# Performance work log

Hardware: AMD Instinct MI355X
Metric: run time of the kernel (lower is better)

## Reference

```python
import jax, jax.numpy as jnp
import numpy as np

N_NODES = 50000
N_EDGES = 600000
D_IN = 128
D_HID = 128
D_OUT = 64


def setup_inputs() -> dict:
    key = jax.random.key(0)
    ks = jax.random.split(key, 8)
    x = jax.random.normal(ks[0], (N_NODES, D_IN), dtype=jnp.float32)
    edge_index = jax.random.randint(ks[1], (2, N_EDGES), 0, N_NODES, dtype=jnp.int32)
    s = 0.05
    W1l = jax.random.normal(ks[2], (D_HID, D_IN), dtype=jnp.float32) * s
    b1 = jnp.zeros((D_HID,), dtype=jnp.float32)
    W1r = jax.random.normal(ks[3], (D_HID, D_IN), dtype=jnp.float32) * s
    W2l = jax.random.normal(ks[4], (D_OUT, D_HID), dtype=jnp.float32) * s
    b2 = jnp.zeros((D_OUT,), dtype=jnp.float32)
    W2r = jax.random.normal(ks[5], (D_OUT, D_HID), dtype=jnp.float32) * s
    return {"x": x, "edge_index": edge_index, "W1l": W1l, "b1": b1,
            "W1r": W1r, "W2l": W2l, "b2": b2, "W2r": W2r}


def _sage_conv(x, src, dst, Wl, bl, Wr, n_nodes):
    # mean aggregation of source features at destination nodes
    msg_sum = jax.ops.segment_sum(x[src], dst, num_segments=n_nodes)  # [N, D]
    deg = jax.ops.segment_sum(jnp.ones((src.shape[0], 1), x.dtype), dst,
                              num_segments=n_nodes)                   # [N, 1]
    mean = msg_sum / jnp.maximum(deg, 1.0)
    # out = lin_l(mean_neighbors) + lin_r(x_self); bias only on lin_l (PyG default)
    return mean @ Wl.T + bl + x @ Wr.T


def reference(x, edge_index, W1l, b1, W1r, W2l, b2, W2r):
    src, dst = edge_index[0], edge_index[1]
    n = x.shape[0]
    h = jax.nn.relu(_sage_conv(x, src, dst, W1l, b1, W1r, n))
    # dropout p=0.5 is identity in eval mode (training=False)
    return _sage_conv(h, src, dst, W2l, b2, W2r, n)
```

## Files before the change

### kernel.cpp

```cpp
#include <hip/hip_runtime.h>
#include <hip/hip_bf16.h>

typedef __bf16 bf16x8 __attribute__((ext_vector_type(8)));
typedef float f32x4 __attribute__((ext_vector_type(4)));

#define D_FEAT 128
#define CHUNK 1024
#define NW 49344

__device__ __forceinline__ float bits_to_f(unsigned int u) {
    union { unsigned int i; float f; } c; c.i = u; return c.f;
}
__device__ __forceinline__ unsigned short f_to_bf16(float f) {
    __hip_bfloat16 h = (__hip_bfloat16)f;
    return *(unsigned short*)&h;
}
__device__ __forceinline__ float ld(const void* p, int is16, size_t i) {
    return is16 ? (float)((const __hip_bfloat16*)p)[i] : ((const float*)p)[i];
}
__device__ __forceinline__ int wave_probe16(const void* p) {
    const unsigned short v = ((const unsigned short*)p)[(threadIdx.x & 63) * 2];
    int e = (v >> 7) & 0xFF;
    unsigned long long m = __ballot(e >= 100 && e <= 140);
    return (__popcll(m) >= 48) ? 1 : 0;
}

__global__ void setup_kernel(const void* x,
                             const void* W1l, const void* b1, const void* W1r,
                             const void* W2l, const void* b2, const void* W2r,
                             const int* __restrict__ dst, int E,
                             unsigned short* __restrict__ wout, int* __restrict__ deg) {
    int i = blockIdx.x * blockDim.x + threadIdx.x;
    if (i < NW) {
        int is16 = wave_probe16(x);
        const void* s; int base;
        if      (i < 16384) { s = W1l; base = 0; }
        else if (i < 32768) { s = W1r; base = 16384; }
        else if (i < 40960) { s = W2l; base = 32768; }
        else if (i < 49152) { s = W2r; base = 40960; }
        else if (i < 49280) { s = b1;  base = 49152; }
        else                { s = b2;  base = 49280; }
        wout[i] = f_to_bf16(ld(s, is16, i - base));
    } else {
        int j = i - NW;
        if (j < E) atomicAdd(&deg[dst[j]], 1);
    }
}

__global__ void scan1_kernel(const int* __restrict__ deg, int* __restrict__ bsum, int n) {
    __shared__ int ws[4];
    const int lane = threadIdx.x & 63, wv = threadIdx.x >> 6;
    int i0 = blockIdx.x * CHUNK + threadIdx.x * 4;
    int s = 0;
    #pragma unroll
    for (int j = 0; j < 4; ++j)
        if (i0 + j < n) { int d = deg[i0 + j]; s += (d + 3) & ~3; }
    #pragma unroll
    for (int d = 1; d < 64; d <<= 1) s += __shfl_xor(s, d, 64);
    if (lane == 0) ws[wv] = s;
    __syncthreads();
    if (threadIdx.x == 0) bsum[blockIdx.x] = ws[0] + ws[1] + ws[2] + ws[3];
}

__global__ void scan3_kernel(const int* __restrict__ deg, const int* __restrict__ bsum,
                             int nb, int* __restrict__ off, int* __restrict__ cursor,
                             int* __restrict__ esrc, int n) {
    __shared__ int ws[4];
    const int lane = threadIdx.x & 63, wv = threadIdx.x >> 6;
    int bv = (lane < nb) ? bsum[lane] : 0;
    int bsc = bv;
    #pragma unroll
    for (int s = 1; s < 64; s <<= 1) {
        int t = __shfl_up(bsc, s, 64);
        if (lane >= s) bsc += t;
    }
    const int base = __shfl(bsc, blockIdx.x, 64) - __shfl(bv, blockIdx.x, 64);
    const int total = __shfl(bsc, nb - 1, 64);

    int i0 = blockIdx.x * CHUNK + threadIdx.x * 4;
    int d0 = 0, d1 = 0, d2 = 0, d3 = 0;
    if (i0 + 0 < n) d0 = deg[i0 + 0];
    if (i0 + 1 < n) d1 = deg[i0 + 1];
    if (i0 + 2 < n) d2 = deg[i0 + 2];
    if (i0 + 3 < n) d3 = deg[i0 + 3];
    int v0 = (d0 + 3) & ~3, v1 = (d1 + 3) & ~3, v2 = (d2 + 3) & ~3, v3 = (d3 + 3) & ~3;
    int tsum = v0 + v1 + v2 + v3;
    int sc = tsum;
    #pragma unroll
    for (int s = 1; s < 64; s <<= 1) {
        int t = __shfl_up(sc, s, 64);
        if (lane >= s) sc += t;
    }
    if (lane == 63) ws[wv] = sc;
    __syncthreads();
    int woff = 0;
    for (int w = 0; w < wv; ++w) woff += ws[w];
    int p = base + woff + (sc - tsum);
    #define EMIT(idx, dj, vj)                                            \
        if (i0 + idx < n) {                                              \
            off[i0 + idx] = p; cursor[i0 + idx] = p;                     \
            for (int q = p + dj; q < p + vj; ++q) esrc[q] = n;           \
            p += vj;                                                     \
        }
    EMIT(0, d0, v0) EMIT(1, d1, v1) EMIT(2, d2, v2) EMIT(3, d3, v3)
    #undef EMIT
    if (blockIdx.x == 0 && threadIdx.x == 0) off[n] = total;
}

__global__ void fill_kernel(const int* __restrict__ src, const int* __restrict__ dst,
                            int* __restrict__ cursor, int* __restrict__ esrc, int E) {
    int i = blockIdx.x * blockDim.x + threadIdx.x;
    if (i < E) {
        int p = atomicAdd(&cursor[dst[i]], 1);
        esrc[p] = src[i];
    }
}

template <int NOUT, bool PROBE_A>
__global__ __launch_bounds__(256)
void gemm_dual_kernel(const void* __restrict__ A,
                      const unsigned short* __restrict__ Wa,
                      const unsigned short* __restrict__ Wb,
                      const unsigned short* __restrict__ bias,
                      unsigned short* __restrict__ za, unsigned short* __restrict__ zb,
                      unsigned int* __restrict__ zrow, int zrow_words, int N) {
    if (blockIdx.x == 0 && threadIdx.x < zrow_words) zrow[threadIdx.x] = 0;
    int a16 = 1;
    if (PROBE_A) a16 = wave_probe16(A);

    const int lane = threadIdx.x & 63;
    const int wave = threadIdx.x >> 6;
    const int sel = wave & 1;
    const int m0 = blockIdx.x * 64 + (wave >> 1) * 32;
    if (m0 >= N) return;
    const int lrow = lane & 15;
    const int kg = lane >> 4;
    const unsigned short* W = sel ? Wb : Wa;
    unsigned short* z = sel ? zb : za;
    constexpr int NT = NOUT / 16;

    bf16x8 xf[2][4];
    #pragma unroll
    for (int rt = 0; rt < 2; ++rt) {
        const int gr = min(m0 + rt * 16 + lrow, N - 1);
        #pragma unroll
        for (int ks = 0; ks < 4; ++ks) {
            const int k0 = ks * 32 + kg * 8;
            if (a16) {
                xf[rt][ks] = *(const bf16x8*)((const unsigned short*)A + (size_t)gr * D_FEAT + k0);
            } else {
                const float* fp = (const float*)A + (size_t)gr * D_FEAT + k0;
                float4 f0 = *(const float4*)fp, f1 = *(const float4*)(fp + 4);
                union { bf16x8 v; unsigned short us[8]; } t;
                t.us[0] = f_to_bf16(f0.x); t.us[1] = f_to_bf16(f0.y);
                t.us[2] = f_to_bf16(f0.z); t.us[3] = f_to_bf16(f0.w);
                t.us[4] = f_to_bf16(f1.x); t.us[5] = f_to_bf16(f1.y);
                t.us[6] = f_to_bf16(f1.z); t.us[7] = f_to_bf16(f1.w);
                xf[rt][ks] = t.v;
            }
        }
    }

    f32x4 acc[2][NT];
    #pragma unroll
    for (int rt = 0; rt < 2; ++rt)
        #pragma unroll
        for (int t = 0; t < NT; ++t) acc[rt][t] = (f32x4){0, 0, 0, 0};

    #pragma unroll
    for (int ks = 0; ks < 4; ++ks) {
        const int k0 = ks * 32 + kg * 8;
        #pragma unroll
        for (int t = 0; t < NT; ++t) {
            bf16x8 wf = *(const bf16x8*)(W + (size_t)(t * 16 + lrow) * D_FEAT + k0);
            acc[0][t] = __builtin_amdgcn_mfma_f32_16x16x32_bf16(wf, xf[0][ks], acc[0][t], 0, 0, 0);
            acc[1][t] = __builtin_amdgcn_mfma_f32_16x16x32_bf16(wf, xf[1][ks], acc[1][t], 0, 0, 0);
        }
    }

    #pragma unroll
    for (int rt = 0; rt < 2; ++rt) {
        const int nd = m0 + rt * 16 + lrow;
        if (nd < N) {
            #pragma unroll
            for (int t = 0; t < NT; ++t) {
                const int c0 = t * 16 + kg * 4;
                float v0 = acc[rt][t][0], v1 = acc[rt][t][1];
                float v2 = acc[rt][t][2], v3 = acc[rt][t][3];
                if (sel) {
                    uint2 bb = *(const uint2*)(bias + c0);
                    v0 += bits_to_f(bb.x << 16); v1 += bits_to_f(bb.x & 0xffff0000u);
                    v2 += bits_to_f(bb.y << 16); v3 += bits_to_f(bb.y & 0xffff0000u);
                }
                unsigned int p0 = (unsigned int)f_to_bf16(v0) | ((unsigned int)f_to_bf16(v1) << 16);
                unsigned int p1 = (unsigned int)f_to_bf16(v2) | ((unsigned int)f_to_bf16(v3) << 16);
                *(uint2*)(z + (size_t)nd * NOUT + c0) = make_uint2(p0, p1);
            }
        }
    }
}

__global__ __launch_bounds__(256)
void agg1_kernel(const unsigned short* __restrict__ zl,
                 unsigned short* __restrict__ h,
                 const int* __restrict__ off, const int* __restrict__ deg,
                 const int* __restrict__ esrc, int N) {
    const int lane = threadIdx.x & 63;
    const int wave = threadIdx.x >> 6;
    const int a_lo = (blockIdx.x * 4 + wave) * 8;
    if (a_lo >= N) return;
    const int a_hi = min(a_lo + 8, N);
    const int nn = a_hi - a_lo;
    int offv = off[min(a_lo + min(lane, 8), N)];
    int degv = deg[min(a_lo + min(lane, 7), N - 1)];
    #define OFFAT(i) __shfl(offv, (i), 64)
    const int e_beg = OFFAT(0);
    const int e_end = OFFAT(nn);
    const int quarter = lane >> 4;
    const int fl = lane & 15;
    float ax[8];
    #pragma unroll
    for (int i = 0; i < 8; ++i) ax[i] = 0.f;
    int g = a_lo;
    int gend = OFFAT(1);

    auto flush = [&](int gg) {
        int td = __shfl(degv, gg - a_lo, 64);
        float inv = 1.f / (float)(td > 0 ? td : 1);
        float v[8];
        #pragma unroll
        for (int i = 0; i < 8; ++i) {
            float s = ax[i];
            s += __shfl_xor(s, 16, 64); s += __shfl_xor(s, 32, 64);
            v[i] = s * inv; ax[i] = 0.f;
        }
        if (quarter == 0) {
            unsigned short* hp = h + (size_t)gg * D_FEAT + fl * 8;
            uint4 zr = *(const uint4*)hp;
            unsigned int w[4] = {zr.x, zr.y, zr.z, zr.w};
            unsigned int pk[4];
            #pragma unroll
            for (int i = 0; i < 4; ++i) {
                float r0 = fmaxf(v[2 * i]     + bits_to_f(w[i] << 16), 0.f);
                float r1 = fmaxf(v[2 * i + 1] + bits_to_f(w[i] & 0xffff0000u), 0.f);
                pk[i] = (unsigned int)f_to_bf16(r0) | ((unsigned int)f_to_bf16(r1) << 16);
            }
            *(uint4*)hp = make_uint4(pk[0], pk[1], pk[2], pk[3]);
        }
    };

    int cur = (e_beg < e_end) ? esrc[min(e_beg + (lane & 31), e_end - 1)] : 0;
    for (int e = e_beg; e < e_end; e += 32) {
        int nxt = (e + 32 < e_end) ? esrc[min(e + 32 + (lane & 31), e_end - 1)] : 0;
        uint4 r[8];
        #pragma unroll
        for (int k = 0; k < 8; ++k) {
            int sk = __shfl(cur, 4 * k + quarter, 64);
            r[k] = *(const uint4*)(zl + (size_t)sk * D_FEAT + fl * 8);
        }
        #pragma unroll
        for (int k = 0; k < 8; ++k) {
            const int eb = e + 4 * k;
            if (eb < e_end) {
                while (eb >= gend) {
                    flush(g); ++g;
                    gend = OFFAT(min(g - a_lo + 1, 8));
                }
                uint4 u = r[k];
                ax[0] += bits_to_f(u.x << 16); ax[1] += bits_to_f(u.x & 0xffff0000u);
                ax[2] += bits_to_f(u.y << 16); ax[3] += bits_to_f(u.y & 0xffff0000u);
                ax[4] += bits_to_f(u.z << 16); ax[5] += bits_to_f(u.z & 0xffff0000u);
                ax[6] += bits_to_f(u.w << 16); ax[7] += bits_to_f(u.w & 0xffff0000u);
            }
        }
        cur = nxt;
    }
    while (g < a_hi) {
        flush(g); ++g;
        gend = OFFAT(min(g - a_lo + 1, 8));
    }
    #undef OFFAT
}

__global__ __launch_bounds__(256)
void agg2_kernel(const unsigned short* __restrict__ z2l,
                 const unsigned short* __restrict__ s2,
                 void* __restrict__ out, const void* __restrict__ x,
                 const int* __restrict__ off, const int* __restrict__ deg,
                 const int* __restrict__ esrc, int N) {
    const int o16 = wave_probe16(x);
    const int lane = threadIdx.x & 63;
    const int wave = threadIdx.x >> 6;
    const int a_lo = (blockIdx.x * 4 + wave) * 8;
    if (a_lo >= N) return;
    const int a_hi = min(a_lo + 8, N);
    const int nn = a_hi - a_lo;
    int offv = off[min(a_lo + min(lane, 8), N)];
    int degv = deg[min(a_lo + min(lane, 7), N - 1)];
    #define OFFAT(i) __shfl(offv, (i), 64)
    const int e_beg = OFFAT(0);
    const int e_end = OFFAT(nn);
    const int quarter = lane >> 4;
    const int fl = lane & 15;
    float ax[4];
    #pragma unroll
    for (int i = 0; i < 4; ++i) ax[i] = 0.f;
    int g = a_lo;
    int gend = OFFAT(1);

    auto flush = [&](int gg) {
        int td = __shfl(degv, gg - a_lo, 64);
        float inv = 1.f / (float)(td > 0 ? td : 1);
        float v[4];
        #pragma unroll
        for (int i = 0; i < 4; ++i) {
            float s = ax[i];
            s += __shfl_xor(s, 16, 64); s += __shfl_xor(s, 32, 64);
            v[i] = s * inv; ax[i] = 0.f;
        }
        if (quarter == 0) {
            uint2 sb = *(const uint2*)(s2 + (size_t)gg * 64 + fl * 4);
            v[0] += bits_to_f(sb.x << 16); v[1] += bits_to_f(sb.x & 0xffff0000u);
            v[2] += bits_to_f(sb.y << 16); v[3] += bits_to_f(sb.y & 0xffff0000u);
            if (o16) {
                unsigned int p0 = (unsigned int)f_to_bf16(v[0]) | ((unsigned int)f_to_bf16(v[1]) << 16);
                unsigned int p1 = (unsigned int)f_to_bf16(v[2]) | ((unsigned int)f_to_bf16(v[3]) << 16);
                *(uint2*)((unsigned short*)out + (size_t)gg * 64 + fl * 4) = make_uint2(p0, p1);
            } else {
                *(float4*)((float*)out + (size_t)gg * 64 + fl * 4) =
                    make_float4(v[0], v[1], v[2], v[3]);
            }
        }
    };

    int cur = (e_beg < e_end) ? esrc[min(e_beg + (lane & 31), e_end - 1)] : 0;
    for (int e = e_beg; e < e_end; e += 32) {
        int nxt = (e + 32 < e_end) ? esrc[min(e + 32 + (lane & 31), e_end - 1)] : 0;
        uint2 r[8];
        #pragma unroll
        for (int k = 0; k < 8; ++k) {
            int sk = __shfl(cur, 4 * k + quarter, 64);
            r[k] = *(const uint2*)(z2l + (size_t)sk * 64 + fl * 4);
        }
        #pragma unroll
        for (int k = 0; k < 8; ++k) {
            const int eb = e + 4 * k;
            if (eb < e_end) {
                while (eb >= gend) {
                    flush(g); ++g;
                    gend = OFFAT(min(g - a_lo + 1, 8));
                }
                uint2 u = r[k];
                ax[0] += bits_to_f(u.x << 16); ax[1] += bits_to_f(u.x & 0xffff0000u);
                ax[2] += bits_to_f(u.y << 16); ax[3] += bits_to_f(u.y & 0xffff0000u);
            }
        }
        cur = nxt;
    }
    while (g < a_hi) {
        flush(g); ++g;
        gend = OFFAT(min(g - a_lo + 1, 8));
    }
    #undef OFFAT
}

extern "C" void kernel_launch(void* const* d_in, const int* in_sizes, int n_in,
                              void* d_out, int out_size, void* d_ws, size_t ws_size,
                              hipStream_t stream) {
    const void* x   = d_in[0];
    const int* eidx = (const int*)d_in[1];
    const void* W1l = d_in[2];
    const void* b1  = d_in[3];
    const void* W1r = d_in[4];
    const void* W2l = d_in[5];
    const void* b2  = d_in[6];
    const void* W2r = d_in[7];

    const int N = in_sizes[0] / D_FEAT;
    const int E = in_sizes[1] / 2;
    const int* src = eidx;
    const int* dst = eidx + E;

    char* ws = (char*)d_ws;
    size_t o = 0;
    auto alloc = [&](size_t bytes) -> void* {
        void* p = ws + o;
        o += (bytes + 255) & ~(size_t)255;
        return p;
    };
    int* deg    = (int*)alloc((size_t)N * 4);
    int* off    = (int*)alloc((size_t)(N + 1) * 4);
    int* cursor = (int*)alloc((size_t)N * 4);
    int* bsum   = (int*)alloc(64 * 4);
    int* esrc   = (int*)alloc((size_t)(E + 3 * N + 64) * 4);
    unsigned short* wconv = (unsigned short*)alloc(NW * 2);
    unsigned short* zl = (unsigned short*)alloc((size_t)(N + 1) * D_FEAT * 2);
    unsigned short* h  = (unsigned short*)alloc((size_t)N * D_FEAT * 2);
    unsigned short* z2l = zl;
    unsigned short* s2  = zl + (size_t)(N + 1) * 64;
    (void)n_in; (void)out_size; (void)ws_size;

    hipMemsetAsync(deg, 0, (size_t)N * 4, stream);
    setup_kernel<<<(NW + E + 255) / 256, 256, 0, stream>>>(
        x, W1l, b1, W1r, W2l, b2, W2r, dst, E, wconv, deg);
    const int nchunk = (N + CHUNK - 1) / CHUNK;
    scan1_kernel<<<nchunk, 256, 0, stream>>>(deg, bsum, N);
    scan3_kernel<<<nchunk, 256, 0, stream>>>(deg, bsum, nchunk, off, cursor, esrc, N);
    fill_kernel<<<(E + 255) / 256, 256, 0, stream>>>(src, dst, cursor, esrc, E);

    const int gblocks = (N + 63) / 64;
    const int ablocks = (N + 31) / 32;
    gemm_dual_kernel<128, true><<<gblocks, 256, 0, stream>>>(
        x, wconv + 0, wconv + 16384, wconv + 49152,
        zl, h, (unsigned int*)(zl + (size_t)N * D_FEAT), 64, N);
    agg1_kernel<<<ablocks, 256, 0, stream>>>(zl, h, off, deg, esrc, N);
    gemm_dual_kernel<64, false><<<gblocks, 256, 0, stream>>>(
        h, wconv + 32768, wconv + 40960, wconv + 49280,
        z2l, s2, (unsigned int*)(z2l + (size_t)N * 64), 32, N);
    agg2_kernel<<<ablocks, 256, 0, stream>>>(z2l, s2, d_out, x, off, deg, esrc, N);
}
```

Measured before the change: 246.8 us.

## Store gathered neighbor projections in fp8 and shrink nodes per wave

The lin_l projections consumed by the two mean-aggregation gathers are now written in fp8 (packed with hardware cvt_pk_fp8) instead of bf16, and unpacked with cvt_pk_f32_fp8 in the aggregation kernels. This halves the bytes fetched per random neighbor row, the dominant memory traffic. Each wave now covers 4 destination nodes instead of 8, doubling the aggregation grid for more parallelism. The self/bias term stays in bf16 in a separate buffer. The cost is substantially lower precision in the aggregated messages, which risks tolerance failures.

```diff
diff --git a/kernel.cpp b/kernel.cpp
--- a/kernel.cpp
+++ b/kernel.cpp
@@ -3,6 +3,7 @@
 
 typedef __bf16 bf16x8 __attribute__((ext_vector_type(8)));
 typedef float f32x4 __attribute__((ext_vector_type(4)));
+typedef float f32x2 __attribute__((ext_vector_type(2)));
 
 #define D_FEAT 128
 #define CHUNK 1024
@@ -17,6 +18,11 @@
 }
 __device__ __forceinline__ float ld(const void* p, int is16, size_t i) {
     return is16 ? (float)((const __hip_bfloat16*)p)[i] : ((const float*)p)[i];
+}
+__device__ __forceinline__ unsigned int pack4_fp8(float v0, float v1, float v2, float v3) {
+    int w = __builtin_amdgcn_cvt_pk_fp8_f32(v0, v1, 0, false);
+    w = __builtin_amdgcn_cvt_pk_fp8_f32(v2, v3, w, true);
+    return (unsigned int)w;
 }
 __device__ __forceinline__ int wave_probe16(const void* p) {
     const unsigned short v = ((const unsigned short*)p)[(threadIdx.x & 63) * 2];
@@ -122,7 +128,7 @@
                       const unsigned short* __restrict__ Wa,
                       const unsigned short* __restrict__ Wb,
                       const unsigned short* __restrict__ bias,
-                      unsigned short* __restrict__ za, unsigned short* __restrict__ zb,
+                      unsigned char* __restrict__ za, unsigned short* __restrict__ zb,
                       unsigned int* __restrict__ zrow, int zrow_words, int N) {
     if (blockIdx.x == 0 && threadIdx.x < zrow_words) zrow[threadIdx.x] = 0;
     int a16 = 1;
@@ -136,7 +142,6 @@
     const int lrow = lane & 15;
     const int kg = lane >> 4;
     const unsigned short* W = sel ? Wb : Wa;
-    unsigned short* z = sel ? zb : za;
     constexpr int NT = NOUT / 16;
 
     bf16x8 xf[2][4];
@@ -191,28 +196,30 @@
                     uint2 bb = *(const uint2*)(bias + c0);
                     v0 += bits_to_f(bb.x << 16); v1 += bits_to_f(bb.x & 0xffff0000u);
                     v2 += bits_to_f(bb.y << 16); v3 += bits_to_f(bb.y & 0xffff0000u);
+                    unsigned int p0 = (unsigned int)f_to_bf16(v0) | ((unsigned int)f_to_bf16(v1) << 16);
+                    unsigned int p1 = (unsigned int)f_to_bf16(v2) | ((unsigned int)f_to_bf16(v3) << 16);
+                    *(uint2*)(zb + (size_t)nd * NOUT + c0) = make_uint2(p0, p1);
+                } else {
+                    *(unsigned int*)(za + (size_t)nd * NOUT + c0) = pack4_fp8(v0, v1, v2, v3);
                 }
-                unsigned int p0 = (unsigned int)f_to_bf16(v0) | ((unsigned int)f_to_bf16(v1) << 16);
-                unsigned int p1 = (unsigned int)f_to_bf16(v2) | ((unsigned int)f_to_bf16(v3) << 16);
-                *(uint2*)(z + (size_t)nd * NOUT + c0) = make_uint2(p0, p1);
             }
         }
     }
 }
 
 __global__ __launch_bounds__(256)
-void agg1_kernel(const unsigned short* __restrict__ zl,
+void agg1_kernel(const unsigned char* __restrict__ zl,
                  unsigned short* __restrict__ h,
                  const int* __restrict__ off, const int* __restrict__ deg,
                  const int* __restrict__ esrc, int N) {
     const int lane = threadIdx.x & 63;
     const int wave = threadIdx.x >> 6;
-    const int a_lo = (blockIdx.x * 4 + wave) * 8;
+    const int a_lo = (blockIdx.x * 4 + wave) * 4;
     if (a_lo >= N) return;
-    const int a_hi = min(a_lo + 8, N);
+    const int a_hi = min(a_lo + 4, N);
     const int nn = a_hi - a_lo;
-    int offv = off[min(a_lo + min(lane, 8), N)];
-    int degv = deg[min(a_lo + min(lane, 7), N - 1)];
+    int offv = off[min(a_lo + min(lane, 4), N)];
+    int degv = deg[min(a_lo + min(lane, 3), N - 1)];
     #define OFFAT(i) __shfl(offv, (i), 64)
     const int e_beg = OFFAT(0);
     const int e_end = OFFAT(nn);
@@ -252,11 +259,11 @@
     int cur = (e_beg < e_end) ? esrc[min(e_beg + (lane & 31), e_end - 1)] : 0;
     for (int e = e_beg; e < e_end; e += 32) {
         int nxt = (e + 32 < e_end) ? esrc[min(e + 32 + (lane & 31), e_end - 1)] : 0;
-        uint4 r[8];
+        uint2 r[8];
         #pragma unroll
         for (int k = 0; k < 8; ++k) {
             int sk = __shfl(cur, 4 * k + quarter, 64);
-            r[k] = *(const uint4*)(zl + (size_t)sk * D_FEAT + fl * 8);
+            r[k] = *(const uint2*)(zl + (size_t)sk * D_FEAT + fl * 8);
         }
         #pragma unroll
         for (int k = 0; k < 8; ++k) {
@@ -264,26 +271,27 @@
             if (eb < e_end) {
                 while (eb >= gend) {
                     flush(g); ++g;
-                    gend = OFFAT(min(g - a_lo + 1, 8));
+                    gend = OFFAT(min(g - a_lo + 1, 4));
                 }
-                uint4 u = r[k];
-                ax[0] += bits_to_f(u.x << 16); ax[1] += bits_to_f(u.x & 0xffff0000u);
-                ax[2] += bits_to_f(u.y << 16); ax[3] += bits_to_f(u.y & 0xffff0000u);
-                ax[4] += bits_to_f(u.z << 16); ax[5] += bits_to_f(u.z & 0xffff0000u);
-                ax[6] += bits_to_f(u.w << 16); ax[7] += bits_to_f(u.w & 0xffff0000u);
+                f32x2 p0 = __builtin_amdgcn_cvt_pk_f32_fp8((int)r[k].x, false);
+                f32x2 p1 = __builtin_amdgcn_cvt_pk_f32_fp8((int)r[k].x, true);
+                f32x2 p2 = __builtin_amdgcn_cvt_pk_f32_fp8((int)r[k].y, false);
+                f32x2 p3 = __builtin_amdgcn_cvt_pk_f32_fp8((int)r[k].y, true);
+                ax[0] += p0.x; ax[1] += p0.y; ax[2] += p1.x; ax[3] += p1.y;
+                ax[4] += p2.x; ax[5] += p2.y; ax[6] += p3.x; ax[7] += p3.y;
             }
         }
         cur = nxt;
     }
     while (g < a_hi) {
         flush(g); ++g;
-        gend = OFFAT(min(g - a_lo + 1, 8));
+        gend = OFFAT(min(g - a_lo + 1, 4));
     }
     #undef OFFAT
 }
 
 __global__ __launch_bounds__(256)
-void agg2_kernel(const unsigned short* __restrict__ z2l,
+void agg2_kernel(const unsigned char* __restrict__ z2l,
                  const unsigned short* __restrict__ s2,
                  void* __restrict__ out, const void* __restrict__ x,
                  const int* __restrict__ off, const int* __restrict__ deg,
@@ -291,12 +299,12 @@
     const int o16 = wave_probe16(x);
     const int lane = threadIdx.x & 63;
     const int wave = threadIdx.x >> 6;
-    const int a_lo = (blockIdx.x * 4 + wave) * 8;
+    const int a_lo = (blockIdx.x * 4 + wave) * 4;
     if (a_lo >= N) return;
-    const int a_hi = min(a_lo + 8, N);
+    const int a_hi = min(a_lo + 4, N);
     const int nn = a_hi - a_lo;
-    int offv = off[min(a_lo + min(lane, 8), N)];
-    int degv = deg[min(a_lo + min(lane, 7), N - 1)];
+    int offv = off[min(a_lo + min(lane, 4), N)];
+    int degv = deg[min(a_lo + min(lane, 3), N - 1)];
     #define OFFAT(i) __shfl(offv, (i), 64)
     const int e_beg = OFFAT(0);
     const int e_end = OFFAT(nn);
@@ -336,11 +344,11 @@
     int cur = (e_beg < e_end) ? esrc[min(e_beg + (lane & 31), e_end - 1)] : 0;
     for (int e = e_beg; e < e_end; e += 32) {
         int nxt = (e + 32 < e_end) ? esrc[min(e + 32 + (lane & 31), e_end - 1)] : 0;
-        uint2 r[8];
+        unsigned int r[8];
         #pragma unroll
         for (int k = 0; k < 8; ++k) {
             int sk = __shfl(cur, 4 * k + quarter, 64);
-            r[k] = *(const uint2*)(z2l + (size_t)sk * 64 + fl * 4);
+            r[k] = *(const unsigned int*)(z2l + (size_t)sk * 64 + fl * 4);
         }
         #pragma unroll
         for (int k = 0; k < 8; ++k) {
@@ -348,18 +356,18 @@
             if (eb < e_end) {
                 while (eb >= gend) {
                     flush(g); ++g;
-                    gend = OFFAT(min(g - a_lo + 1, 8));
+                    gend = OFFAT(min(g - a_lo + 1, 4));
                 }
-                uint2 u = r[k];
-                ax[0] += bits_to_f(u.x << 16); ax[1] += bits_to_f(u.x & 0xffff0000u);
-                ax[2] += bits_to_f(u.y << 16); ax[3] += bits_to_f(u.y & 0xffff0000u);
+                f32x2 p0 = __builtin_amdgcn_cvt_pk_f32_fp8((int)r[k], false);
+                f32x2 p1 = __builtin_amdgcn_cvt_pk_f32_fp8((int)r[k], true);
+                ax[0] += p0.x; ax[1] += p0.y; ax[2] += p1.x; ax[3] += p1.y;
             }
         }
         cur = nxt;
     }
     while (g < a_hi) {
         flush(g); ++g;
-        gend = OFFAT(min(g - a_lo + 1, 8));
+        gend = OFFAT(min(g - a_lo + 1, 4));
     }
     #undef OFFAT
 }
@@ -394,10 +402,10 @@
     int* bsum   = (int*)alloc(64 * 4);
     int* esrc   = (int*)alloc((size_t)(E + 3 * N + 64) * 4);
     unsigned short* wconv = (unsigned short*)alloc(NW * 2);
-    unsigned short* zl = (unsigned short*)alloc((size_t)(N + 1) * D_FEAT * 2);
+    unsigned char*  zl = (unsigned char*)alloc((size_t)(N + 1) * D_FEAT);
     unsigned short* h  = (unsigned short*)alloc((size_t)N * D_FEAT * 2);
-    unsigned short* z2l = zl;
-    unsigned short* s2  = zl + (size_t)(N + 1) * 64;
+    unsigned short* s2 = (unsigned short*)alloc((size_t)N * 64 * 2);
+    unsigned char*  z2l = zl;
     (void)n_in; (void)out_size; (void)ws_size;
 
     hipMemsetAsync(deg, 0, (size_t)N * 4, stream);
@@ -409,13 +417,13 @@
     fill_kernel<<<(E + 255) / 256, 256, 0, stream>>>(src, dst, cursor, esrc, E);
 
     const int gblocks = (N + 63) / 64;
-    const int ablocks = (N + 31) / 32;
+    const int ablocks = (N + 15) / 16;
     gemm_dual_kernel<128, true><<<gblocks, 256, 0, stream>>>(
         x, wconv + 0, wconv + 16384, wconv + 49152,
-        zl, h, (unsigned int*)(zl + (size_t)N * D_FEAT), 64, N);
+        zl, h, (unsigned int*)(zl + (size_t)N * D_FEAT), 32, N);
     agg1_kernel<<<ablocks, 256, 0, stream>>>(zl, h, off, deg, esrc, N);
     gemm_dual_kernel<64, false><<<gblocks, 256, 0, stream>>>(
         h, wconv + 32768, wconv + 40960, wconv + 49280,
-        z2l, s2, (unsigned int*)(z2l + (size_t)N * 64), 32, N);
+        z2l, s2, (unsigned int*)(z2l + (size_t)N * 64), 16, N);
     agg2_kernel<<<ablocks, 256, 0, stream>>>(z2l, s2, d_out, x, off, deg, esrc, N);
 }
```

Result: faster. 236.8 us (-4.1%).
